# Kernel optimization log

Hardware: AMD Instinct MI355X
Metric: run time of the kernel (lower is better)

Reference implementation:

```python
import jax, jax.numpy as jnp
import numpy as np

VOCAB = 50257
NSAMPLES = 1048576


def setup_inputs() -> dict:
    key = jax.random.key(0)
    k1, k2 = jax.random.split(key)
    # positive sampling weights (need not be normalized, as in WeightedRandomSampler)
    frequencies = jax.random.uniform(k1, (VOCAB,), dtype=jnp.float32) + 1e-3
    # pre-drawn uniforms, one per sample (replacement=True => iid draws)
    u = jax.random.uniform(k2, (NSAMPLES,), dtype=jnp.float32)
    return {"frequencies": frequencies, "u": u}


def reference(frequencies, u):
    # WeightedRandomSampler with replacement == multinomial sampling proportional
    # to frequencies. Implemented as inverse-CDF: normalize, cumsum, binary search.
    cdf = jnp.cumsum(frequencies)          # [V], unnormalized CDF
    total = cdf[-1]
    # scale uniforms into [0, total) instead of dividing the whole CDF (fewer ops)
    idx = jnp.searchsorted(cdf, u * total, side="right")  # [N] int indices
    idx = jnp.clip(idx, 0, frequencies.shape[0] - 1)
    # original returns a FloatTensor of the sampled indices
    return idx.astype(jnp.float32)
```

## Files before the change

### kernel.cpp

```cpp
#include <hip/hip_runtime.h>
#include <math.h>


#define TPB 512
#define SPT 8
#define GRP 16
#define GPT_MAX 16

__device__ __forceinline__ int physIdx(int i) { return i + (i >> 5); }

template <int PAD>
__global__ __launch_bounds__(TPB) void sampler_kernel(const float* __restrict__ freq,
                                                      const float* __restrict__ u,
                                                      float* __restrict__ out,
                                                      int N, int V, int G) {
    __shared__ float sS[PAD + (PAD >> 5)];
    __shared__ float wsum[TPB / 64];
    const int t = threadIdx.x;
    const int lane = t & 63;
    const int w = t >> 6;

    const int GPT = (G + TPB - 1) / TPB;
    const int g0 = t * GPT;

    float ls[GPT_MAX];
    float runv = 0.f;
#pragma unroll
    for (int k = 0; k < GPT_MAX; ++k) {
        float s = 0.f;
        if (k < GPT) {
            const int g = g0 + k;
            if (g < G) {
                const int base = g * GRP;
                if (base + GRP <= V) {
                    const float4* fp = reinterpret_cast<const float4*>(freq + base);
                    const float4 a = fp[0], b = fp[1], c = fp[2], d = fp[3];
                    s = a.x; s += a.y; s += a.z; s += a.w;
                    s += b.x; s += b.y; s += b.z; s += b.w;
                    s += c.x; s += c.y; s += c.z; s += c.w;
                    s += d.x; s += d.y; s += d.z; s += d.w;
                } else {
                    for (int j = 0; j < GRP; ++j) {
                        const int idx = base + j;
                        if (idx < V) s += freq[idx];
                    }
                }
            }
        }
        runv += s;
        ls[k] = runv;
    }

    float sc = runv;
#pragma unroll
    for (int off = 1; off <= 32; off <<= 1) {
        const float v = __shfl_up(sc, off);
        if (lane >= off) sc += v;
    }
    if (lane == 63) wsum[w] = sc;
    __syncthreads();
    float tbase = sc - runv;
    for (int k = 0; k < w; ++k) tbase += wsum[k];

#pragma unroll
    for (int k = 0; k < GPT_MAX; ++k) {
        if (k < GPT) {
            const int g = g0 + k;
            if (g < G) sS[physIdx(g)] = tbase + ls[k];
        }
    }
    for (int i = G + t; i < PAD; i += TPB) sS[physIdx(i)] = INFINITY;
    __syncthreads();

    const float total = sS[physIdx(G - 1)];

    const int gid = blockIdx.x * TPB + t;
    const long long i0 = (long long)gid * SPT;
    if (i0 >= N) return;

    float uk[SPT];
    if (i0 + SPT <= N) {
        const float4 A = *reinterpret_cast<const float4*>(u + i0);
        const float4 B = *reinterpret_cast<const float4*>(u + i0 + 4);
        uk[0] = A.x; uk[1] = A.y; uk[2] = A.z; uk[3] = A.w;
        uk[4] = B.x; uk[5] = B.y; uk[6] = B.z; uk[7] = B.w;
    } else {
#pragma unroll
        for (int s = 0; s < SPT; ++s) uk[s] = (i0 + s < N) ? u[i0 + s] : 0.f;
    }

    float ok[SPT];
#pragma unroll
    for (int s = 0; s < SPT; ++s) {
        const float key = uk[s] * total;

        int pos = -1;
#pragma unroll
        for (int step = PAD >> 1; step >= 1; step >>= 1) {
            const int j = pos + step;
            pos += (sS[physIdx(j)] <= key) ? step : 0;
        }
        int g = pos + 1;
        g = (g > G - 1) ? (G - 1) : g;
        const float base = (g > 0) ? sS[physIdx(g - 1)] : 0.f;
        const int eb = g * GRP;

        float r = base;
        int cnt = 0;
        if (eb + GRP <= V) {
            const float4* fp = reinterpret_cast<const float4*>(freq + eb);
            const float4 a = fp[0], b = fp[1], c = fp[2], d = fp[3];
            r += a.x; cnt += (r <= key); r += a.y; cnt += (r <= key);
            r += a.z; cnt += (r <= key); r += a.w; cnt += (r <= key);
            r += b.x; cnt += (r <= key); r += b.y; cnt += (r <= key);
            r += b.z; cnt += (r <= key); r += b.w; cnt += (r <= key);
            r += c.x; cnt += (r <= key); r += c.y; cnt += (r <= key);
            r += c.z; cnt += (r <= key); r += c.w; cnt += (r <= key);
            r += d.x; cnt += (r <= key); r += d.y; cnt += (r <= key);
            r += d.z; cnt += (r <= key); r += d.w; cnt += (r <= key);
        } else {
            for (int j = 0; j < GRP; ++j) {
                const int idx = eb + j;
                if (idx < V) { r += freq[idx]; cnt += (r <= key); }
            }
        }
        int ans = eb + cnt;
        ans = (ans > V - 1) ? (V - 1) : ans;
        ok[s] = (float)ans;
    }

    if (i0 + SPT <= N) {
        *reinterpret_cast<float4*>(out + i0)     = make_float4(ok[0], ok[1], ok[2], ok[3]);
        *reinterpret_cast<float4*>(out + i0 + 4) = make_float4(ok[4], ok[5], ok[6], ok[7]);
    } else {
        for (int s = 0; s < SPT; ++s)
            if (i0 + s < N) out[i0 + s] = ok[s];
    }
}

extern "C" void kernel_launch(void* const* d_in, const int* in_sizes, int n_in,
                              void* d_out, int out_size, void* d_ws, size_t ws_size,
                              hipStream_t stream) {
    const float* freq = (const float*)d_in[0];
    const float* u    = (const float*)d_in[1];
    float* out        = (float*)d_out;
    const int V = in_sizes[0];
    const int N = in_sizes[1];
    const int G = (V + GRP - 1) / GRP;
    const int NB = (N + TPB * SPT - 1) / (TPB * SPT);

    if (G < 1024) {
        hipLaunchKernelGGL(sampler_kernel<1024>, dim3(NB), dim3(TPB), 0, stream,
                           freq, u, out, N, V, G);
    } else if (G < 2048) {
        hipLaunchKernelGGL(sampler_kernel<2048>, dim3(NB), dim3(TPB), 0, stream,
                           freq, u, out, N, V, G);
    } else if (G < 4096) {
        hipLaunchKernelGGL(sampler_kernel<4096>, dim3(NB), dim3(TPB), 0, stream,
                           freq, u, out, N, V, G);
    } else {
        hipLaunchKernelGGL(sampler_kernel<8192>, dim3(NB), dim3(TPB), 0, stream,
                           freq, u, out, N, V, G);
    }
}
```

Measured before the change: 19.33 us.

## Precompute group sums in separate kernel and replace binary search with LUT

```diff
diff --git a/kernel.cpp b/kernel.cpp
--- a/kernel.cpp
+++ b/kernel.cpp
@@ -2,55 +2,58 @@
 #include <math.h>
 
 
+#define GRP 16
 #define TPB 512
-#define SPT 8
-#define GRP 16
-#define GPT_MAX 16
+#define SPT 4
+#define GPT_MAX 8
+#define KLUT 8192
+#define GMAX 4096
 
-__device__ __forceinline__ int physIdx(int i) { return i + (i >> 5); }
+__global__ __launch_bounds__(256) void gsum_kernel(const float* __restrict__ freq,
+                                                   int V, float* __restrict__ gsum) {
+    const int i4 = blockIdx.x * 256 + threadIdx.x;
+    const int nf4 = (V + 3) >> 2;
+    float s = 0.f;
+    if (i4 < nf4) {
+        const int base = i4 * 4;
+        if (base + 3 < V) {
+            const float4 v = *reinterpret_cast<const float4*>(freq + base);
+            s = v.x + v.y + v.z + v.w;
+        } else {
+            for (int j = 0; j < 4; ++j)
+                if (base + j < V) s += freq[base + j];
+        }
+    }
+    s += __shfl_xor(s, 1);
+    s += __shfl_xor(s, 2);
+    const int g = i4 >> 2;
+    const int G = (V + GRP - 1) / GRP;
+    if ((threadIdx.x & 3) == 0 && g < G) gsum[g] = s;
+}
 
-template <int PAD>
-__global__ __launch_bounds__(TPB) void sampler_kernel(const float* __restrict__ freq,
-                                                      const float* __restrict__ u,
-                                                      float* __restrict__ out,
-                                                      int N, int V, int G) {
-    __shared__ float sS[PAD + (PAD >> 5)];
+__global__ __launch_bounds__(TPB) void sample_kernel(const float* __restrict__ freq,
+                                                     const float* __restrict__ u,
+                                                     const float* __restrict__ gsum,
+                                                     float* __restrict__ out,
+                                                     int N, int V, int G) {
+    __shared__ float cdfS[GMAX];
+    __shared__ unsigned short lut[KLUT + 1];
     __shared__ float wsum[TPB / 64];
     const int t = threadIdx.x;
     const int lane = t & 63;
     const int w = t >> 6;
+    const int GPT = (G + TPB - 1) / TPB;
 
-    const int GPT = (G + TPB - 1) / TPB;
     const int g0 = t * GPT;
-
     float ls[GPT_MAX];
     float runv = 0.f;
 #pragma unroll
     for (int k = 0; k < GPT_MAX; ++k) {
         float s = 0.f;
-        if (k < GPT) {
-            const int g = g0 + k;
-            if (g < G) {
-                const int base = g * GRP;
-                if (base + GRP <= V) {
-                    const float4* fp = reinterpret_cast<const float4*>(freq + base);
-                    const float4 a = fp[0], b = fp[1], c = fp[2], d = fp[3];
-                    s = a.x; s += a.y; s += a.z; s += a.w;
-                    s += b.x; s += b.y; s += b.z; s += b.w;
-                    s += c.x; s += c.y; s += c.z; s += c.w;
-                    s += d.x; s += d.y; s += d.z; s += d.w;
-                } else {
-                    for (int j = 0; j < GRP; ++j) {
-                        const int idx = base + j;
-                        if (idx < V) s += freq[idx];
-                    }
-                }
-            }
-        }
+        if (k < GPT) { const int g = g0 + k; if (g < G) s = gsum[g]; }
         runv += s;
         ls[k] = runv;
     }
-
     float sc = runv;
 #pragma unroll
     for (int off = 1; off <= 32; off <<= 1) {
@@ -64,15 +67,36 @@
 
 #pragma unroll
     for (int k = 0; k < GPT_MAX; ++k) {
-        if (k < GPT) {
-            const int g = g0 + k;
-            if (g < G) sS[physIdx(g)] = tbase + ls[k];
+        if (k < GPT) { const int g = g0 + k; if (g < G) cdfS[g] = tbase + ls[k]; }
+    }
+    for (int b = t; b <= KLUT; b += TPB) {
+        int gg = (int)(((long long)b * G) >> 13);
+        lut[b] = (unsigned short)((gg > G - 1) ? (G - 1) : gg);
+    }
+    __syncthreads();
+
+    const float total = cdfS[G - 1];
+    const float fK = (float)KLUT;
+
+    {
+        float cprev = tbase;
+#pragma unroll
+        for (int k = 0; k < GPT_MAX; ++k) {
+            if (k < GPT) {
+                const int g = g0 + k;
+                if (g < G) {
+                    const float ccur = tbase + ls[k];
+                    int bl = (int)ceilf(fK * (cprev / total));
+                    int bh = (int)ceilf(fK * (ccur / total));
+                    bl = bl < 0 ? 0 : (bl > KLUT ? KLUT : bl);
+                    bh = bh < 0 ? 0 : (bh > KLUT ? KLUT : bh);
+                    for (int b = bl; b < bh; ++b) lut[b] = (unsigned short)g;
+                    cprev = ccur;
+                }
+            }
         }
     }
-    for (int i = G + t; i < PAD; i += TPB) sS[physIdx(i)] = INFINITY;
     __syncthreads();
-
-    const float total = sS[physIdx(G - 1)];
 
     const int gid = blockIdx.x * TPB + t;
     const long long i0 = (long long)gid * SPT;
@@ -81,9 +105,7 @@
     float uk[SPT];
     if (i0 + SPT <= N) {
         const float4 A = *reinterpret_cast<const float4*>(u + i0);
-        const float4 B = *reinterpret_cast<const float4*>(u + i0 + 4);
         uk[0] = A.x; uk[1] = A.y; uk[2] = A.z; uk[3] = A.w;
-        uk[4] = B.x; uk[5] = B.y; uk[6] = B.z; uk[7] = B.w;
     } else {
 #pragma unroll
         for (int s = 0; s < SPT; ++s) uk[s] = (i0 + s < N) ? u[i0 + s] : 0.f;
@@ -93,31 +115,28 @@
 #pragma unroll
     for (int s = 0; s < SPT; ++s) {
         const float key = uk[s] * total;
-
-        int pos = -1;
-#pragma unroll
-        for (int step = PAD >> 1; step >= 1; step >>= 1) {
-            const int j = pos + step;
-            pos += (sS[physIdx(j)] <= key) ? step : 0;
-        }
-        int g = pos + 1;
+        int b = (int)(uk[s] * fK);
+        b = b < 0 ? 0 : (b > KLUT - 1 ? KLUT - 1 : b);
+        int g = lut[b];
         g = (g > G - 1) ? (G - 1) : g;
-        const float base = (g > 0) ? sS[physIdx(g - 1)] : 0.f;
+        while (g < G - 1 && cdfS[g] <= key) ++g;
+        while (g > 0 && cdfS[g - 1] > key) --g;
+        const float base = (g > 0) ? cdfS[g - 1] : 0.f;
         const int eb = g * GRP;
 
         float r = base;
         int cnt = 0;
         if (eb + GRP <= V) {
             const float4* fp = reinterpret_cast<const float4*>(freq + eb);
-            const float4 a = fp[0], b = fp[1], c = fp[2], d = fp[3];
-            r += a.x; cnt += (r <= key); r += a.y; cnt += (r <= key);
-            r += a.z; cnt += (r <= key); r += a.w; cnt += (r <= key);
-            r += b.x; cnt += (r <= key); r += b.y; cnt += (r <= key);
-            r += b.z; cnt += (r <= key); r += b.w; cnt += (r <= key);
-            r += c.x; cnt += (r <= key); r += c.y; cnt += (r <= key);
-            r += c.z; cnt += (r <= key); r += c.w; cnt += (r <= key);
-            r += d.x; cnt += (r <= key); r += d.y; cnt += (r <= key);
-            r += d.z; cnt += (r <= key); r += d.w; cnt += (r <= key);
+            const float4 a = fp[0], bb = fp[1], c = fp[2], d = fp[3];
+            r += a.x;  cnt += (r <= key); r += a.y;  cnt += (r <= key);
+            r += a.z;  cnt += (r <= key); r += a.w;  cnt += (r <= key);
+            r += bb.x; cnt += (r <= key); r += bb.y; cnt += (r <= key);
+            r += bb.z; cnt += (r <= key); r += bb.w; cnt += (r <= key);
+            r += c.x;  cnt += (r <= key); r += c.y;  cnt += (r <= key);
+            r += c.z;  cnt += (r <= key); r += c.w;  cnt += (r <= key);
+            r += d.x;  cnt += (r <= key); r += d.y;  cnt += (r <= key);
+            r += d.z;  cnt += (r <= key); r += d.w;  cnt += (r <= key);
         } else {
             for (int j = 0; j < GRP; ++j) {
                 const int idx = eb + j;
@@ -130,8 +149,7 @@
     }
 
     if (i0 + SPT <= N) {
-        *reinterpret_cast<float4*>(out + i0)     = make_float4(ok[0], ok[1], ok[2], ok[3]);
-        *reinterpret_cast<float4*>(out + i0 + 4) = make_float4(ok[4], ok[5], ok[6], ok[7]);
+        *reinterpret_cast<float4*>(out + i0) = make_float4(ok[0], ok[1], ok[2], ok[3]);
     } else {
         for (int s = 0; s < SPT; ++s)
             if (i0 + s < N) out[i0 + s] = ok[s];
@@ -147,19 +165,14 @@
     const int V = in_sizes[0];
     const int N = in_sizes[1];
     const int G = (V + GRP - 1) / GRP;
+
+    float* gsum = (float*)d_ws;
+
+    const int nf4 = (V + 3) >> 2;
+    hipLaunchKernelGGL(gsum_kernel, dim3((nf4 + 255) / 256), dim3(256), 0, stream,
+                       freq, V, gsum);
+
     const int NB = (N + TPB * SPT - 1) / (TPB * SPT);
-
-    if (G < 1024) {
-        hipLaunchKernelGGL(sampler_kernel<1024>, dim3(NB), dim3(TPB), 0, stream,
-                           freq, u, out, N, V, G);
-    } else if (G < 2048) {
-        hipLaunchKernelGGL(sampler_kernel<2048>, dim3(NB), dim3(TPB), 0, stream,
-                           freq, u, out, N, V, G);
-    } else if (G < 4096) {
-        hipLaunchKernelGGL(sampler_kernel<4096>, dim3(NB), dim3(TPB), 0, stream,
-                           freq, u, out, N, V, G);
-    } else {
-        hipLaunchKernelGGL(sampler_kernel<8192>, dim3(NB), dim3(TPB), 0, stream,
-                           freq, u, out, N, V, G);
-    }
+    hipLaunchKernelGGL(sample_kernel, dim3(NB), dim3(TPB), 0, stream,
+                       freq, u, gsum, out, N, V, G);
 }
```

Measured after the change: 22.61 us. +17.0%, slower.

## Precompute group sums in a separate kernel and halve samples per thread

Applied to the files above, without the earlier changes.

```diff
diff --git a/kernel.cpp b/kernel.cpp
--- a/kernel.cpp
+++ b/kernel.cpp
@@ -2,55 +2,70 @@
 #include <math.h>
 
 
+#define GRP 16
 #define TPB 512
-#define SPT 8
-#define GRP 16
+#define SPT 4
 #define GPT_MAX 16
 
 __device__ __forceinline__ int physIdx(int i) { return i + (i >> 5); }
 
+__global__ __launch_bounds__(256) void gsum_kernel(const float* __restrict__ freq,
+                                                   int V, float* __restrict__ gsum) {
+    const int i4 = blockIdx.x * 256 + threadIdx.x;
+    const int nf4 = (V + 3) >> 2;
+    float s = 0.f;
+    if (i4 < nf4) {
+        const int base = i4 * 4;
+        if (base + 3 < V) {
+            const float4 v = *reinterpret_cast<const float4*>(freq + base);
+            s = v.x + v.y + v.z + v.w;
+        } else {
+            for (int j = 0; j < 4; ++j)
+                if (base + j < V) s += freq[base + j];
+        }
+    }
+    s += __shfl_xor(s, 1);
+    s += __shfl_xor(s, 2);
+    const int g = i4 >> 2;
+    const int G = (V + GRP - 1) / GRP;
+    if ((threadIdx.x & 3) == 0 && g < G) gsum[g] = s;
+}
+
 template <int PAD>
-__global__ __launch_bounds__(TPB) void sampler_kernel(const float* __restrict__ freq,
-                                                      const float* __restrict__ u,
-                                                      float* __restrict__ out,
-                                                      int N, int V, int G) {
+__global__ __launch_bounds__(TPB) void sample_kernel(const float* __restrict__ freq,
+                                                     const float* __restrict__ u,
+                                                     const float* __restrict__ gsum,
+                                                     float* __restrict__ out,
+                                                     int N, int V, int G) {
     __shared__ float sS[PAD + (PAD >> 5)];
     __shared__ float wsum[TPB / 64];
     const int t = threadIdx.x;
     const int lane = t & 63;
     const int w = t >> 6;
+    const int GPT = (G + TPB - 1) / TPB;
 
-    const int GPT = (G + TPB - 1) / TPB;
+    const int gid = blockIdx.x * TPB + t;
+    const long long i0 = (long long)gid * SPT;
+    float uk[SPT];
+    const bool full = (i0 + SPT <= N);
+    if (full) {
+        const float4 A = *reinterpret_cast<const float4*>(u + i0);
+        uk[0] = A.x; uk[1] = A.y; uk[2] = A.z; uk[3] = A.w;
+    } else {
+#pragma unroll
+        for (int s = 0; s < SPT; ++s) uk[s] = (i0 + s < N) ? u[i0 + s] : 0.f;
+    }
+
     const int g0 = t * GPT;
-
     float ls[GPT_MAX];
     float runv = 0.f;
 #pragma unroll
     for (int k = 0; k < GPT_MAX; ++k) {
         float s = 0.f;
-        if (k < GPT) {
-            const int g = g0 + k;
-            if (g < G) {
-                const int base = g * GRP;
-                if (base + GRP <= V) {
-                    const float4* fp = reinterpret_cast<const float4*>(freq + base);
-                    const float4 a = fp[0], b = fp[1], c = fp[2], d = fp[3];
-                    s = a.x; s += a.y; s += a.z; s += a.w;
-                    s += b.x; s += b.y; s += b.z; s += b.w;
-                    s += c.x; s += c.y; s += c.z; s += c.w;
-                    s += d.x; s += d.y; s += d.z; s += d.w;
-                } else {
-                    for (int j = 0; j < GRP; ++j) {
-                        const int idx = base + j;
-                        if (idx < V) s += freq[idx];
-                    }
-                }
-            }
-        }
+        if (k < GPT) { const int g = g0 + k; if (g < G) s = gsum[g]; }
         runv += s;
         ls[k] = runv;
     }
-
     float sc = runv;
 #pragma unroll
     for (int off = 1; off <= 32; off <<= 1) {
@@ -64,30 +79,14 @@
 
 #pragma unroll
     for (int k = 0; k < GPT_MAX; ++k) {
-        if (k < GPT) {
-            const int g = g0 + k;
-            if (g < G) sS[physIdx(g)] = tbase + ls[k];
-        }
+        if (k < GPT) { const int g = g0 + k; if (g < G) sS[physIdx(g)] = tbase + ls[k]; }
     }
     for (int i = G + t; i < PAD; i += TPB) sS[physIdx(i)] = INFINITY;
     __syncthreads();
 
-    const float total = sS[physIdx(G - 1)];
-
-    const int gid = blockIdx.x * TPB + t;
-    const long long i0 = (long long)gid * SPT;
     if (i0 >= N) return;
 
-    float uk[SPT];
-    if (i0 + SPT <= N) {
-        const float4 A = *reinterpret_cast<const float4*>(u + i0);
-        const float4 B = *reinterpret_cast<const float4*>(u + i0 + 4);
-        uk[0] = A.x; uk[1] = A.y; uk[2] = A.z; uk[3] = A.w;
-        uk[4] = B.x; uk[5] = B.y; uk[6] = B.z; uk[7] = B.w;
-    } else {
-#pragma unroll
-        for (int s = 0; s < SPT; ++s) uk[s] = (i0 + s < N) ? u[i0 + s] : 0.f;
-    }
+    const float total = sS[physIdx(G - 1)];
 
     float ok[SPT];
 #pragma unroll
@@ -129,9 +128,8 @@
         ok[s] = (float)ans;
     }
 
-    if (i0 + SPT <= N) {
-        *reinterpret_cast<float4*>(out + i0)     = make_float4(ok[0], ok[1], ok[2], ok[3]);
-        *reinterpret_cast<float4*>(out + i0 + 4) = make_float4(ok[4], ok[5], ok[6], ok[7]);
+    if (full) {
+        *reinterpret_cast<float4*>(out + i0) = make_float4(ok[0], ok[1], ok[2], ok[3]);
     } else {
         for (int s = 0; s < SPT; ++s)
             if (i0 + s < N) out[i0 + s] = ok[s];
@@ -147,19 +145,25 @@
     const int V = in_sizes[0];
     const int N = in_sizes[1];
     const int G = (V + GRP - 1) / GRP;
+
+    float* gsum = (float*)d_ws;
+
+    const int nf4 = (V + 3) >> 2;
+    hipLaunchKernelGGL(gsum_kernel, dim3((nf4 + 255) / 256), dim3(256), 0, stream,
+                       freq, V, gsum);
+
     const int NB = (N + TPB * SPT - 1) / (TPB * SPT);
-
     if (G < 1024) {
-        hipLaunchKernelGGL(sampler_kernel<1024>, dim3(NB), dim3(TPB), 0, stream,
-                           freq, u, out, N, V, G);
+        hipLaunchKernelGGL(sample_kernel<1024>, dim3(NB), dim3(TPB), 0, stream,
+                           freq, u, gsum, out, N, V, G);
     } else if (G < 2048) {
-        hipLaunchKernelGGL(sampler_kernel<2048>, dim3(NB), dim3(TPB), 0, stream,
-                           freq, u, out, N, V, G);
+        hipLaunchKernelGGL(sample_kernel<2048>, dim3(NB), dim3(TPB), 0, stream,
+                           freq, u, gsum, out, N, V, G);
     } else if (G < 4096) {
-        hipLaunchKernelGGL(sampler_kernel<4096>, dim3(NB), dim3(TPB), 0, stream,
-                           freq, u, out, N, V, G);
+        hipLaunchKernelGGL(sample_kernel<4096>, dim3(NB), dim3(TPB), 0, stream,
+                           freq, u, gsum, out, N, V, G);
     } else {
-        hipLaunchKernelGGL(sampler_kernel<8192>, dim3(NB), dim3(TPB), 0, stream,
-                           freq, u, out, N, V, G);
+        hipLaunchKernelGGL(sample_kernel<8192>, dim3(NB), dim3(TPB), 0, stream,
+                           freq, u, gsum, out, N, V, G);
     }
 }
```

Result: slower. 19.83 us (+2.6%).
